# Optimization experiments

Hardware: AMD Instinct MI355X
Metric: run time of the kernel (lower is better)

The kernel has to match this reference:

```python
import jax, jax.numpy as jnp
import numpy as np

EMBED_DIM = 1024
NUM_HEADS = 16
CONTEXT = 250
MAX_PERIOD = 10000.0
HEAD_DIM = EMBED_DIM // NUM_HEADS


def setup_inputs() -> dict:
    key = jax.random.key(0)
    k1, k2, k3 = jax.random.split(key, 3)
    B, T = 2, 2048
    query = jax.random.normal(k1, (B, T, EMBED_DIM), jnp.float32)
    in_proj_w = jax.random.normal(k2, (3 * EMBED_DIM, EMBED_DIM), jnp.float32) * (EMBED_DIM ** -0.5)
    out_proj_w = jax.random.normal(k3, (EMBED_DIM, EMBED_DIM), jnp.float32) * (EMBED_DIM ** -0.5)
    return {"query": query, "in_proj_w": in_proj_w, "out_proj_w": out_proj_w}


def _apply_rope(q, k):
    # q, k: [B, H, T, D]; Mimi/Moshi-style interleaved-pair rotary embedding
    B, H, T, D = q.shape
    ds = jnp.arange(D // 2, dtype=jnp.float32)
    freqs = jnp.exp(ds * (-np.log(MAX_PERIOD) * 2.0 / D))  # [D/2]
    ts = jnp.arange(T, dtype=jnp.float32)
    ang = ts[:, None] * freqs[None, :]  # [T, D/2]
    cos = jnp.cos(ang)
    sin = jnp.sin(ang)

    def rot(x):
        xr = x.reshape(B, H, T, D // 2, 2)
        xa, xb = xr[..., 0], xr[..., 1]
        ya = xa * cos - xb * sin
        yb = xa * sin + xb * cos
        return jnp.stack([ya, yb], axis=-1).reshape(B, H, T, D)

    return rot(q), rot(k)


def reference(query, in_proj_w, out_proj_w):
    B, T, E = query.shape
    H, D = NUM_HEADS, HEAD_DIM
    # fused QKV projection (no bias)
    proj = query @ in_proj_w.T  # [B, T, 3E]
    qkv = proj.reshape(B, T, 3, H, D)
    q = jnp.transpose(qkv[:, :, 0], (0, 2, 1, 3))  # [B, H, T, D]
    k = jnp.transpose(qkv[:, :, 1], (0, 2, 1, 3))
    v = jnp.transpose(qkv[:, :, 2], (0, 2, 1, 3))
    q, k = _apply_rope(q, k)
    # causal sliding-window mask: attend iff 0 <= (t_q - t_k) < CONTEXT
    pos = jnp.arange(T)
    delta = pos[:, None] - pos[None, :]  # [T, T]
    mask = (delta >= 0) & (delta < CONTEXT)
    scores = jnp.einsum('bhtd,bhsd->bhts', q, k) * (D ** -0.5)
    scores = jnp.where(mask[None, None, :, :], scores, jnp.finfo(scores.dtype).min)
    attn = jax.nn.softmax(scores, axis=-1)
    x = jnp.einsum('bhts,bhsd->bhtd', attn, v)  # [B, H, T, D]
    x = jnp.transpose(x, (0, 2, 1, 3)).reshape(B, T, E)
    return x @ out_proj_w.T
```

## Files before the change

kernel.cpp:

```cpp
#include <hip/hip_runtime.h>

#define TT 2048
#define EMB 1024
#define NH 16
#define HD 64
#define CTX 250

typedef __attribute__((ext_vector_type(4))) float f32x4;
typedef __attribute__((ext_vector_type(8))) short s16x8;
typedef __attribute__((ext_vector_type(4))) short s16x4;

#define LDS_PTR(p) ((__attribute__((address_space(3))) void*)(p))
#define GLB_PTR(p) ((const __attribute__((address_space(1))) void*)(p))

__device__ __forceinline__ short f2bf(float f) {
  union { float f; unsigned u; } v; v.f = f;
  unsigned r = v.u + 0x7fffu + ((v.u >> 16) & 1u);
  return (short)(r >> 16);
}
__device__ __forceinline__ float bf2f(unsigned short u) {
  union { unsigned u; float f; } v; v.u = ((unsigned)u) << 16;
  return v.f;
}

__global__ void cvt_all(const float* __restrict__ q, const float* __restrict__ wi,
                        const float* __restrict__ wo, short* __restrict__ qo,
                        short* __restrict__ wio, short* __restrict__ woo) {
  int i = blockIdx.x * blockDim.x + threadIdx.x;
  const float* src; short* dst; int off;
  if (i < 1048576)      { src = q;  dst = qo;  off = i; }
  else if (i < 1835008) { src = wi; dst = wio; off = i - 1048576; }
  else                  { src = wo; dst = woo; off = i - 1835008; }
  float4 v = reinterpret_cast<const float4*>(src)[off];
  s16x4 o; o[0] = f2bf(v.x); o[1] = f2bf(v.y); o[2] = f2bf(v.z); o[3] = f2bf(v.w);
  *reinterpret_cast<s16x4*>(dst + off * 4) = o;
}

template<int BM, int LX, int LY, bool BF16OUT>
__global__ __launch_bounds__(256) void gemm_swz(const short* __restrict__ A,
                                                const short* __restrict__ W,
                                                void* __restrict__ Cv, int N, int K) {
  constexpr int BK = 32;
  constexpr int MFR = BM / 32;
  __shared__ __align__(16) short As[BM * BK];
  __shared__ __align__(16) short Bs[128 * BK];
  const int lane = threadIdx.x & 63;
  const int wid  = threadIdx.x >> 6;
  const int lr = lane & 15, lg = lane >> 4;
  const int xcd = blockIdx.x & 7;
  const int sub = blockIdx.x >> 3;
  const int bx = (sub % LX) + LX * (xcd & 1);
  const int by = (sub / LX) + LY * (xcd >> 1);
  const int rblk = by * BM;
  const int cblk = bx * 128;
  const int wrow16 = (wid >> 1) * MFR;
  const int wcol16 = (wid & 1) * 4;
  const int lrow = lane >> 2;
  const int fst  = (lrow & 3) ^ ((lrow >> 2) & 3);
  const int schunk = ((lane & 3) ^ fst) * 8;
  const int frd = (lr & 3) ^ ((lr >> 2) & 3);
  const int rd_off = lr * 32 + ((lg ^ frd) * 8);
  f32x4 acc[MFR][4] = {};

  for (int kk = 0; kk < K; kk += BK) {
#pragma unroll
    for (int j = 0; j < BM / 64; j++) {
      int seg = wid * (BM / 64) + j;
      const short* g = A + (size_t)(rblk + seg * 16 + lrow) * K + kk + schunk;
      __builtin_amdgcn_global_load_lds(GLB_PTR(g), LDS_PTR(&As[seg * 512]), 16, 0, 0);
    }
#pragma unroll
    for (int j = 0; j < 2; j++) {
      int seg = wid * 2 + j;
      const short* g = W + (size_t)(cblk + seg * 16 + lrow) * K + kk + schunk;
      __builtin_amdgcn_global_load_lds(GLB_PTR(g), LDS_PTR(&Bs[seg * 512]), 16, 0, 0);
    }
    __syncthreads();
    s16x8 af[MFR], bfr[4];
#pragma unroll
    for (int m = 0; m < MFR; m++)
      af[m] = *reinterpret_cast<const s16x8*>(&As[(wrow16 + m) * 512 + rd_off]);
#pragma unroll
    for (int n = 0; n < 4; n++)
      bfr[n] = *reinterpret_cast<const s16x8*>(&Bs[(wcol16 + n) * 512 + rd_off]);
#pragma unroll
    for (int m = 0; m < MFR; m++)
#pragma unroll
      for (int n = 0; n < 4; n++)
        acc[m][n] = __builtin_amdgcn_mfma_f32_16x16x32_bf16(af[m], bfr[n], acc[m][n], 0, 0, 0);
    __syncthreads();
  }
#pragma unroll
  for (int m = 0; m < MFR; m++)
#pragma unroll
    for (int n = 0; n < 4; n++)
#pragma unroll
      for (int r = 0; r < 4; r++) {
        int row = rblk + (wrow16 + m) * 16 + lg * 4 + r;
        int col = cblk + (wcol16 + n) * 16 + lr;
        float val = acc[m][n][r];
        if constexpr (BF16OUT) ((short*)Cv)[(size_t)row * N + col] = f2bf(val);
        else                   ((float*)Cv)[(size_t)row * N + col] = val;
      }
}

__global__ __launch_bounds__(256) void rope_v2(const short* __restrict__ proj,
                                               short* __restrict__ Qb,
                                               short* __restrict__ Kb,
                                               short* __restrict__ Vt) {
  int tid = threadIdx.x;
  int t0 = blockIdx.x * 64;
  int bh = blockIdx.y;
  int b = bh >> 4, h = bh & 15;
  __shared__ short vtile[64 * 66];
  int i = tid & 31;
  int trow = tid >> 5;
  float freq = __expf(-(float)i * 0.2878231366f);
#pragma unroll
  for (int it = 0; it < 8; ++it) {
    int tl = it * 8 + trow;
    int t = t0 + tl;
    int pbase = (b * TT + t) * 3 * EMB + h * HD + 2 * i;
    unsigned q01 = *reinterpret_cast<const unsigned*>(proj + pbase);
    unsigned k01 = *reinterpret_cast<const unsigned*>(proj + pbase + EMB);
    unsigned v01 = *reinterpret_cast<const unsigned*>(proj + pbase + 2 * EMB);
    float qa = bf2f((unsigned short)(q01 & 0xffff)), qb_ = bf2f((unsigned short)(q01 >> 16));
    float ka = bf2f((unsigned short)(k01 & 0xffff)), kb_ = bf2f((unsigned short)(k01 >> 16));
    float ang = (float)t * freq;
    float s, c;
    sincosf(ang, &s, &c);
    int obase = (bh * TT + t) * HD + 2 * i;
    unsigned qo = ((unsigned)(unsigned short)f2bf(qa * s + qb_ * c) << 16) |
                  (unsigned short)f2bf(qa * c - qb_ * s);
    unsigned ko = ((unsigned)(unsigned short)f2bf(ka * s + kb_ * c) << 16) |
                  (unsigned short)f2bf(ka * c - kb_ * s);
    *reinterpret_cast<unsigned*>(Qb + obase) = qo;
    *reinterpret_cast<unsigned*>(Kb + obase) = ko;
    *reinterpret_cast<unsigned*>(&vtile[tl * 66 + 2 * i]) = v01;
  }
  __syncthreads();
  int d = tid >> 2, toff = (tid & 3) * 16;
  s16x8 o0, o1;
#pragma unroll
  for (int j = 0; j < 8; ++j) {
    o0[j] = vtile[(toff + j) * 66 + d];
    o1[j] = vtile[(toff + 8 + j) * 66 + d];
  }
  size_t vb = (size_t)(bh * HD + d) * TT + t0 + toff;
  *reinterpret_cast<s16x8*>(Vt + vb) = o0;
  *reinterpret_cast<s16x8*>(Vt + vb + 8) = o1;
}

__global__ __launch_bounds__(256) void attn_v4(const short* __restrict__ Qb,
                                               const short* __restrict__ Kb,
                                               const short* __restrict__ Vt,
                                               short* __restrict__ Xout) {
  int tid = threadIdx.x;
  int lane = tid & 63;
  int w = tid >> 6;
  int lr = lane & 15, lg = lane >> 4;
  int id = blockIdx.x;
  int xcd = id & 7;
  int sub = id >> 3;
  int bh = xcd * 4 + (sub >> 5);
  int tblk = (sub & 31) * 64;
  int t0 = tblk + w * 16;
  int b = bh >> 4, h = bh & 15;
  const short* Qp = Qb + bh * TT * HD;
  const char* Kp = (const char*)(Kb + bh * TT * HD);
  const char* Vtp = (const char*)(Vt + bh * HD * TT);
  __shared__ __align__(16) short Ks[32 * 64];
  __shared__ __align__(16) short Vs[64 * 32];
  __shared__ __align__(16) short p_lds[4][16][40];
  s16x8 qf[2];
#pragma unroll
  for (int d2 = 0; d2 < 2; d2++)
    qf[d2] = *reinterpret_cast<const s16x8*>(Qp + (t0 + lr) * HD + d2 * 32 + lg * 8);
  s16x8 ones;
#pragma unroll
  for (int j = 0; j < 8; j++) ones[j] = (short)0x3F80;
  f32x4 of[4] = {};
  f32x4 ofl = {};
  int lo = tblk - (CTX - 1); if (lo < 0) lo = 0;
  int kt_lo = lo & ~31;
  int kt_hi = (tblk + 63) & ~31;
  int krow = w * 8 + (lane >> 3);
  int kcb  = ((lane & 7) * 16) ^ ((krow & 7) << 4);
  int vd   = w * 16 + (lane >> 2);
  int vcb  = ((lane & 3) * 16) ^ (((vd >> 1) & 3) << 4);
  char* ksdst = (char*)Ks + w * 1024 + lane * 16;
  char* vsdst = (char*)Vs + w * 1024 + lane * 16;
  for (int kt = kt_lo; kt <= kt_hi; kt += 32) {
    __builtin_amdgcn_global_load_lds(GLB_PTR(Kp + (kt + krow) * 128 + kcb),
                                     LDS_PTR(ksdst), 16, 0, 0);
    __builtin_amdgcn_global_load_lds(GLB_PTR(Vtp + vd * (TT * 2) + kt * 2 + vcb),
                                     LDS_PTR(vsdst), 16, 0, 0);
    __syncthreads();
    if (kt <= t0 + 15 && kt + 31 >= t0 - (CTX - 1)) {
      f32x4 s2[2];
#pragma unroll
      for (int hh = 0; hh < 2; hh++) {
        int row = hh * 16 + lr;
        f32x4 sa = {};
#pragma unroll
        for (int d2 = 0; d2 < 2; d2++) {
          int cb = (d2 * 64 + lg * 16) ^ ((row & 7) << 4);
          s16x8 kf = *reinterpret_cast<const s16x8*>((const char*)Ks + row * 128 + cb);
          sa = __builtin_amdgcn_mfma_f32_16x16x32_bf16(qf[d2], kf, sa, 0, 0, 0);
        }
        s2[hh] = sa;
      }
#pragma unroll
      for (int r = 0; r < 4; r++) {
        int row = t0 + lg * 4 + r;
#pragma unroll
        for (int hh = 0; hh < 2; hh++) {
          int col = kt + hh * 16 + lr;
          int dl = row - col;
          bool vdm = (dl >= 0) && (dl < CTX);
          float pv = vdm ? __expf(s2[hh][r] * 0.125f) : 0.0f;
          p_lds[w][lg * 4 + r][hh * 16 + lr] = f2bf(pv);
        }
      }
      s16x8 pa = *reinterpret_cast<const s16x8*>(&p_lds[w][lr][lg * 8]);
#pragma unroll
      for (int n = 0; n < 4; n++) {
        int d = n * 16 + lr;
        int cb = (lg * 16) ^ (((d >> 1) & 3) << 4);
        s16x8 vf = *reinterpret_cast<const s16x8*>((const char*)Vs + d * 64 + cb);
        of[n] = __builtin_amdgcn_mfma_f32_16x16x32_bf16(pa, vf, of[n], 0, 0, 0);
      }
      ofl = __builtin_amdgcn_mfma_f32_16x16x32_bf16(pa, ones, ofl, 0, 0, 0);
    }
    __syncthreads();
  }
#pragma unroll
  for (int r = 0; r < 4; r++) {
    float inv = 1.0f / ofl[r];
    int row = t0 + lg * 4 + r;
#pragma unroll
    for (int n = 0; n < 4; n++)
      Xout[(b * TT + row) * EMB + h * HD + n * 16 + lr] = f2bf(of[n][r] * inv);
  }
}

extern "C" void kernel_launch(void* const* d_in, const int* in_sizes, int n_in,
                              void* d_out, int out_size, void* d_ws, size_t ws_size,
                              hipStream_t stream) {
  const float* query = (const float*)d_in[0];
  const float* w_in  = (const float*)d_in[1];
  const float* w_out = (const float*)d_in[2];
  char* ws = (char*)d_ws;
  short* qbf   = (short*)(ws + 0);
  short* wibf  = (short*)(ws + 8388608);
  short* wobf  = (short*)(ws + 14680064);
  short* proj  = (short*)(ws + 16777216);
  short* attnx = (short*)(ws + 16777216);
  short* Qb    = (short*)(ws + 41943040);
  short* Kb    = (short*)(ws + 50331648);
  short* Vt    = (short*)(ws + 58720256);

  cvt_all<<<8192, 256, 0, stream>>>(query, w_in, w_out, qbf, wibf, wobf);
  gemm_swz<128, 12, 8, true><<<768, 256, 0, stream>>>(qbf, wibf, (void*)proj, 3072, 1024);
  rope_v2<<<dim3(32, 32), 256, 0, stream>>>(proj, Qb, Kb, Vt);
  attn_v4<<<1024, 256, 0, stream>>>(Qb, Kb, Vt, attnx);
  gemm_swz<64, 4, 16, false><<<512, 256, 0, stream>>>(attnx, wobf, d_out, 1024, 1024);
}
```

Measured before the change: 97.27 us.

## Fuse RoPE and V transpose into QKV GEMM epilogue using precomputed sin/cos table

Removes the separate rope kernel and the intermediate bf16 projection buffer. The QKV GEMM epilogue now applies the rotary embedding, pairing elements with a lane shuffle, writes Q/K in head-major layout, and writes V transposed. A cos/sin table is built inside the conversion kernel. The generic out-projection GEMM also drops its XOR-swizzled LDS layout for a plain one, which may add LDS bank conflicts. The fused epilogue's scattered 2-byte Q/K stores and 8-byte strided V stores may be less coalesced than before.

```diff
diff --git a/kernel.cpp b/kernel.cpp
--- a/kernel.cpp
+++ b/kernel.cpp
@@ -25,8 +25,22 @@
 
 __global__ void cvt_all(const float* __restrict__ q, const float* __restrict__ wi,
                         const float* __restrict__ wo, short* __restrict__ qo,
-                        short* __restrict__ wio, short* __restrict__ woo) {
+                        short* __restrict__ wio, short* __restrict__ woo,
+                        float2* __restrict__ tbl) {
   int i = blockIdx.x * blockDim.x + threadIdx.x;
+  if (i >= 2097152) {
+    int tix = (i - 2097152) * 4;
+#pragma unroll
+    for (int e = 0; e < 4; ++e) {
+      int idx = tix + e;
+      int t = idx >> 5, fi = idx & 31;
+      float freq = __expf(-(float)fi * 0.2878231366f);
+      float s, c;
+      sincosf((float)t * freq, &s, &c);
+      tbl[idx] = make_float2(c, s);
+    }
+    return;
+  }
   const float* src; short* dst; int off;
   if (i < 1048576)      { src = q;  dst = qo;  off = i; }
   else if (i < 1835008) { src = wi; dst = wio; off = i - 1048576; }
@@ -34,6 +48,98 @@
   float4 v = reinterpret_cast<const float4*>(src)[off];
   s16x4 o; o[0] = f2bf(v.x); o[1] = f2bf(v.y); o[2] = f2bf(v.z); o[3] = f2bf(v.w);
   *reinterpret_cast<s16x4*>(dst + off * 4) = o;
+}
+
+__global__ __launch_bounds__(256) void gemm_qkv(const short* __restrict__ A,
+                                                const short* __restrict__ W,
+                                                short* __restrict__ Qb,
+                                                short* __restrict__ Kb,
+                                                short* __restrict__ Vt,
+                                                const float2* __restrict__ tbl,
+                                                int N, int K) {
+  constexpr int BM = 128, BK = 32, MFR = 4;
+  __shared__ __align__(16) short As[BM * BK];
+  __shared__ __align__(16) short Bs[128 * BK];
+  const int lane = threadIdx.x & 63;
+  const int wid  = threadIdx.x >> 6;
+  const int lr = lane & 15, lg = lane >> 4;
+  const int xcd = blockIdx.x & 7;
+  const int sub = blockIdx.x >> 3;
+  const int bx = (sub % 12) + 12 * (xcd & 1);
+  const int by = (sub / 12) + 8 * (xcd >> 1);
+  const int rblk = by * BM;
+  const int cblk = bx * 128;
+  const int wrow = (wid >> 1) * 64;
+  const int wcol = (wid & 1) * 64;
+  const int lrow = lane >> 2;
+  const int fst  = (lrow & 3) ^ ((lrow >> 2) & 3);
+  const int schunk = ((lane & 3) ^ fst) * 8;
+  const int frd = (lr & 3) ^ ((lr >> 2) & 3);
+  const int rd_off = lr * 32 + ((lg ^ frd) * 8);
+  f32x4 acc[MFR][4] = {};
+
+  for (int kk = 0; kk < K; kk += BK) {
+#pragma unroll
+    for (int j = 0; j < 2; j++) {
+      int seg = wid * 2 + j;
+      const short* g = A + (size_t)(rblk + seg * 16 + lrow) * K + kk + schunk;
+      __builtin_amdgcn_global_load_lds(GLB_PTR(g), LDS_PTR(&As[seg * 512]), 16, 0, 0);
+    }
+#pragma unroll
+    for (int j = 0; j < 2; j++) {
+      int seg = wid * 2 + j;
+      const short* g = W + (size_t)(cblk + seg * 16 + lrow) * K + kk + schunk;
+      __builtin_amdgcn_global_load_lds(GLB_PTR(g), LDS_PTR(&Bs[seg * 512]), 16, 0, 0);
+    }
+    __syncthreads();
+    s16x8 af[MFR], bfr[4];
+#pragma unroll
+    for (int m = 0; m < MFR; m++)
+      af[m] = *reinterpret_cast<const s16x8*>(&As[(wrow / 16 + m) * 512 + rd_off]);
+#pragma unroll
+    for (int n = 0; n < 4; n++)
+      bfr[n] = *reinterpret_cast<const s16x8*>(&Bs[(wcol / 16 + n) * 512 + rd_off]);
+#pragma unroll
+    for (int m = 0; m < MFR; m++)
+#pragma unroll
+      for (int n = 0; n < 4; n++)
+        acc[m][n] = __builtin_amdgcn_mfma_f32_16x16x32_bf16(af[m], bfr[n], acc[m][n], 0, 0, 0);
+    __syncthreads();
+  }
+
+  const int sel = cblk >> 10;
+  const int dcol_base = (cblk & 1023) + wcol;
+#pragma unroll
+  for (int m = 0; m < MFR; m++) {
+    int trow = rblk + wrow + m * 16 + lg * 4;
+    int b = trow >> 11;
+    int tq = trow & 2047;
+#pragma unroll
+    for (int n = 0; n < 4; n++) {
+      int dcol = dcol_base + n * 16 + lr;
+      int h = dcol >> 6;
+      int d = dcol & 63;
+      size_t bh = (size_t)(b * NH + h);
+      if (sel == 2) {
+        s16x4 pk;
+#pragma unroll
+        for (int r = 0; r < 4; r++) pk[r] = f2bf(acc[m][n][r]);
+        *reinterpret_cast<s16x4*>(Vt + (bh * HD + d) * TT + tq) = pk;
+      } else {
+        short* dst = (sel == 0) ? Qb : Kb;
+        const float2* tp = tbl + (size_t)tq * 32 + (d >> 1);
+#pragma unroll
+        for (int r = 0; r < 4; r++) {
+          float val = acc[m][n][r];
+          float oth = __shfl_xor(val, 1);
+          float2 cs = tp[r * 32];
+          float res = (lane & 1) ? (oth * cs.y + val * cs.x)
+                                 : (val * cs.x - oth * cs.y);
+          dst[(bh * TT + tq + r) * HD + d] = f2bf(res);
+        }
+      }
+    }
+  }
 }
 
 template<int BM, int LX, int LY, bool BF16OUT>
@@ -53,36 +159,33 @@
   const int by = (sub / LX) + LY * (xcd >> 1);
   const int rblk = by * BM;
   const int cblk = bx * 128;
-  const int wrow16 = (wid >> 1) * MFR;
-  const int wcol16 = (wid & 1) * 4;
-  const int lrow = lane >> 2;
-  const int fst  = (lrow & 3) ^ ((lrow >> 2) & 3);
-  const int schunk = ((lane & 3) ^ fst) * 8;
-  const int frd = (lr & 3) ^ ((lr >> 2) & 3);
-  const int rd_off = lr * 32 + ((lg ^ frd) * 8);
+  const int wrow = (wid >> 1) * (BM / 2);
+  const int wcol = (wid & 1) * 64;
+  const int srow = lane >> 2;
+  const int scol = (lane & 3) * 8;
   f32x4 acc[MFR][4] = {};
 
   for (int kk = 0; kk < K; kk += BK) {
 #pragma unroll
     for (int j = 0; j < BM / 64; j++) {
       int seg = wid * (BM / 64) + j;
-      const short* g = A + (size_t)(rblk + seg * 16 + lrow) * K + kk + schunk;
+      const short* g = A + (size_t)(rblk + seg * 16 + srow) * K + kk + scol;
       __builtin_amdgcn_global_load_lds(GLB_PTR(g), LDS_PTR(&As[seg * 512]), 16, 0, 0);
     }
 #pragma unroll
     for (int j = 0; j < 2; j++) {
       int seg = wid * 2 + j;
-      const short* g = W + (size_t)(cblk + seg * 16 + lrow) * K + kk + schunk;
+      const short* g = W + (size_t)(cblk + seg * 16 + srow) * K + kk + scol;
       __builtin_amdgcn_global_load_lds(GLB_PTR(g), LDS_PTR(&Bs[seg * 512]), 16, 0, 0);
     }
     __syncthreads();
     s16x8 af[MFR], bfr[4];
 #pragma unroll
     for (int m = 0; m < MFR; m++)
-      af[m] = *reinterpret_cast<const s16x8*>(&As[(wrow16 + m) * 512 + rd_off]);
+      af[m] = *reinterpret_cast<const s16x8*>(&As[(wrow + m * 16 + lr) * BK + lg * 8]);
 #pragma unroll
     for (int n = 0; n < 4; n++)
-      bfr[n] = *reinterpret_cast<const s16x8*>(&Bs[(wcol16 + n) * 512 + rd_off]);
+      bfr[n] = *reinterpret_cast<const s16x8*>(&Bs[(wcol + n * 16 + lr) * BK + lg * 8]);
 #pragma unroll
     for (int m = 0; m < MFR; m++)
 #pragma unroll
@@ -96,59 +199,12 @@
     for (int n = 0; n < 4; n++)
 #pragma unroll
       for (int r = 0; r < 4; r++) {
-        int row = rblk + (wrow16 + m) * 16 + lg * 4 + r;
-        int col = cblk + (wcol16 + n) * 16 + lr;
+        int row = rblk + wrow + m * 16 + lg * 4 + r;
+        int col = cblk + wcol + n * 16 + lr;
         float val = acc[m][n][r];
         if constexpr (BF16OUT) ((short*)Cv)[(size_t)row * N + col] = f2bf(val);
         else                   ((float*)Cv)[(size_t)row * N + col] = val;
       }
-}
-
-__global__ __launch_bounds__(256) void rope_v2(const short* __restrict__ proj,
-                                               short* __restrict__ Qb,
-                                               short* __restrict__ Kb,
-                                               short* __restrict__ Vt) {
-  int tid = threadIdx.x;
-  int t0 = blockIdx.x * 64;
-  int bh = blockIdx.y;
-  int b = bh >> 4, h = bh & 15;
-  __shared__ short vtile[64 * 66];
-  int i = tid & 31;
-  int trow = tid >> 5;
-  float freq = __expf(-(float)i * 0.2878231366f);
-#pragma unroll
-  for (int it = 0; it < 8; ++it) {
-    int tl = it * 8 + trow;
-    int t = t0 + tl;
-    int pbase = (b * TT + t) * 3 * EMB + h * HD + 2 * i;
-    unsigned q01 = *reinterpret_cast<const unsigned*>(proj + pbase);
-    unsigned k01 = *reinterpret_cast<const unsigned*>(proj + pbase + EMB);
-    unsigned v01 = *reinterpret_cast<const unsigned*>(proj + pbase + 2 * EMB);
-    float qa = bf2f((unsigned short)(q01 & 0xffff)), qb_ = bf2f((unsigned short)(q01 >> 16));
-    float ka = bf2f((unsigned short)(k01 & 0xffff)), kb_ = bf2f((unsigned short)(k01 >> 16));
-    float ang = (float)t * freq;
-    float s, c;
-    sincosf(ang, &s, &c);
-    int obase = (bh * TT + t) * HD + 2 * i;
-    unsigned qo = ((unsigned)(unsigned short)f2bf(qa * s + qb_ * c) << 16) |
-                  (unsigned short)f2bf(qa * c - qb_ * s);
-    unsigned ko = ((unsigned)(unsigned short)f2bf(ka * s + kb_ * c) << 16) |
-                  (unsigned short)f2bf(ka * c - kb_ * s);
-    *reinterpret_cast<unsigned*>(Qb + obase) = qo;
-    *reinterpret_cast<unsigned*>(Kb + obase) = ko;
-    *reinterpret_cast<unsigned*>(&vtile[tl * 66 + 2 * i]) = v01;
-  }
-  __syncthreads();
-  int d = tid >> 2, toff = (tid & 3) * 16;
-  s16x8 o0, o1;
-#pragma unroll
-  for (int j = 0; j < 8; ++j) {
-    o0[j] = vtile[(toff + j) * 66 + d];
-    o1[j] = vtile[(toff + 8 + j) * 66 + d];
-  }
-  size_t vb = (size_t)(bh * HD + d) * TT + t0 + toff;
-  *reinterpret_cast<s16x8*>(Vt + vb) = o0;
-  *reinterpret_cast<s16x8*>(Vt + vb + 8) = o1;
 }
 
 __global__ __launch_bounds__(256) void attn_v4(const short* __restrict__ Qb,
@@ -254,15 +310,14 @@
   short* qbf   = (short*)(ws + 0);
   short* wibf  = (short*)(ws + 8388608);
   short* wobf  = (short*)(ws + 14680064);
-  short* proj  = (short*)(ws + 16777216);
-  short* attnx = (short*)(ws + 16777216);
+  float2* tbl  = (float2*)(ws + 16777216);
+  short* attnx = (short*)(ws + 17301504);
   short* Qb    = (short*)(ws + 41943040);
   short* Kb    = (short*)(ws + 50331648);
   short* Vt    = (short*)(ws + 58720256);
 
-  cvt_all<<<8192, 256, 0, stream>>>(query, w_in, w_out, qbf, wibf, wobf);
-  gemm_swz<128, 12, 8, true><<<768, 256, 0, stream>>>(qbf, wibf, (void*)proj, 3072, 1024);
-  rope_v2<<<dim3(32, 32), 256, 0, stream>>>(proj, Qb, Kb, Vt);
+  cvt_all<<<8256, 256, 0, stream>>>(query, w_in, w_out, qbf, wibf, wobf, tbl);
+  gemm_qkv<<<768, 256, 0, stream>>>(qbf, wibf, Qb, Kb, Vt, tbl, 3072, 1024);
   attn_v4<<<1024, 256, 0, stream>>>(Qb, Kb, Vt, attnx);
   gemm_swz<64, 4, 16, false><<<512, 256, 0, stream>>>(attnx, wobf, d_out, 1024, 1024);
 }
```

Result: faster. 93.66 us (-3.7%).
